# Optimization experiments

Measured on AMD Instinct MI355X. Metric: run time of the kernel, lower is better.

The kernel has to match this reference:

```python
import jax, jax.numpy as jnp
import numpy as np

NH, DH = 16, 64          # n_head, d_head
CH = NH + DH             # 80
RQ, RK, RV = 6, 2, 2
ROPE_BASE = 10000.0


def _rotary(b, cache_len):
    # b: [B, T, R, DH]; rotates the d-factor exactly as the torch Rotary module
    T = b.shape[1]
    inv_freq = (1.0 / ROPE_BASE) ** (jnp.arange(0, DH, 2, dtype=jnp.float32) / DH)
    t = jnp.arange(T, dtype=jnp.float32) + cache_len
    freqs = jnp.outer(t, inv_freq)                      # [T, DH/2]
    cos = freqs[None, :, None, :].astype(b.dtype)
    sin = jnp.sin(freqs)[None, :, None, :].astype(b.dtype)
    cos = jnp.cos(freqs)[None, :, None, :].astype(b.dtype)
    x1, x2 = jnp.split(b, 2, axis=3)
    return jnp.concatenate([x1 * cos + x2 * sin, -x1 * sin + x2 * cos], axis=3)


def setup_inputs() -> dict:
    key = jax.random.key(0)
    k1, k2, k3, k4 = jax.random.split(key, 4)
    B, T, D = 2, 2048, 1024
    x = jax.random.normal(k1, (B, T, D), dtype=jnp.float32)
    # xavier-uniform-like scale for factor projections
    s_q = float(np.sqrt(6.0 / (D + CH)))
    s_o = float(np.sqrt(6.0 / (D + D)))
    W_abq = jax.random.uniform(k2, (RQ * CH, D), minval=-s_q, maxval=s_q, dtype=jnp.float32)
    W_abkv = jax.random.uniform(k3, ((RK + RV) * CH, D), minval=-s_q, maxval=s_q, dtype=jnp.float32)
    W_o = jax.random.uniform(k4, (D, D), minval=-s_o, maxval=s_o, dtype=jnp.float32)
    return {"x": x, "W_abq": W_abq, "W_abkv": W_abkv, "W_o": W_o}


def reference(x, W_abq, W_abkv, W_o):
    B, T, D = x.shape
    # low-rank factor projections
    abq = (x @ W_abq.T).reshape(B, T, RQ, CH)
    a_q, b_q = abq[..., :NH], abq[..., NH:]            # [B,T,RQ,NH], [B,T,RQ,DH]
    abkv = (x @ W_abkv.T).reshape(B, T, RK + RV, CH)
    a_kv = abkv[..., :NH]
    b_kv = _rotary(abkv[..., NH:], cache_len=0)        # RoPE applied to K/V d-factors only
    a_k, b_k = a_kv[:, :, :RK], b_kv[:, :, :RK]
    a_v, b_v = a_kv[:, :, RK:], b_kv[:, :, RK:]
    # tensor-product reconstruction of Q/K/V
    q = jnp.einsum('btrh,btrd->bthd', a_q, b_q) / RQ
    k = jnp.einsum('btrh,btrd->bthd', a_k, b_k) / RK
    v = jnp.einsum('btrh,btrd->bthd', a_v, b_v) / RV
    # causal attention (flex_attention default scale = 1/sqrt(dh))
    scale = 1.0 / jnp.sqrt(jnp.asarray(DH, dtype=q.dtype))
    scores = jnp.einsum('bqhd,bkhd->bhqk', q, k) * scale
    causal = jnp.tril(jnp.ones((T, T), dtype=bool))
    scores = jnp.where(causal[None, None], scores, jnp.finfo(scores.dtype).min)
    attn = jax.nn.softmax(scores, axis=-1)
    y = jnp.einsum('bhqk,bkhd->bqhd', attn, v).reshape(B, T, D)
    return y @ W_o.T
```

## Files before the change

kernel.cpp:

```cpp
#include <hip/hip_runtime.h>
#include <hip/hip_bf16.h>
#include <math.h>

#define NHEADS 16
#define DHEAD  64
#define CHDIM  80
#define RQn    6
#define RKn    2
#define RVn    2
#define BB     2
#define TT     2048
#define DDim   1024
#define NQK    800

using frag16 = __attribute__((ext_vector_type(8))) short;
using f32x4  = __attribute__((ext_vector_type(4))) float;
using f32x16 = __attribute__((ext_vector_type(16))) float;

#define AS1(p) ((const __attribute__((address_space(1))) unsigned int*)(p))
#define AS3(p) ((__attribute__((address_space(3))) unsigned int*)(p))

static __device__ __forceinline__ unsigned short bf16_bits(float f) {
    __hip_bfloat16 h = __float2bfloat16(f);
    return *(unsigned short*)&h;
}
static __device__ __forceinline__ unsigned int pk2(float a, float b) {
    return ((unsigned int)bf16_bits(b) << 16) | (unsigned int)bf16_bits(a);
}

__global__ __launch_bounds__(256) void cvt_all(
    const float* __restrict__ x, const float* __restrict__ wq,
    const float* __restrict__ wk, const float* __restrict__ wo,
    __hip_bfloat16* __restrict__ xb, __hip_bfloat16* __restrict__ wqk,
    __hip_bfloat16* __restrict__ wob)
{
    int bid = blockIdx.x;
    const float* src; __hip_bfloat16* dst; int n4;
    if (bid < 4096)      { src = x;  dst = xb;            n4 = 1048576; }
    else if (bid < 4576) { bid -= 4096; src = wq; dst = wqk;           n4 = 122880; }
    else if (bid < 4896) { bid -= 4576; src = wk; dst = wqk + 491520;  n4 = 81920; }
    else                 { bid -= 4896; src = wo; dst = wob;           n4 = 262144; }
    int i = bid * 256 + threadIdx.x;
    if (i < n4) {
        float4 v = *(const float4*)&src[i * 4];
        ushort4 o;
        o.x = bf16_bits(v.x); o.y = bf16_bits(v.y);
        o.z = bf16_bits(v.z); o.w = bf16_bits(v.w);
        *(ushort4*)&dst[i * 4] = o;
    }
}

__global__ __launch_bounds__(256) void gemm_bf16(
    const __hip_bfloat16* __restrict__ A, const __hip_bfloat16* __restrict__ W,
    float* __restrict__ C, int M, int N, int K)
{
    __shared__ __hip_bfloat16 Asl[2][128 * 64];
    __shared__ __hip_bfloat16 Bsl[2][128 * 64];
    const int tid = threadIdx.x;
    const int w = tid >> 6, lane = tid & 63;
    const int l16 = lane & 15, quad = lane >> 4;
    const int wr = w >> 1, wc = w & 1;
    const int bm = blockIdx.y * 128, bn = blockIdx.x * 128;

    int rS[4], cS[4], rBS[4];
    #pragma unroll
    for (int j = 0; j < 4; j++) {
        int L = (w * 4 + j) * 64 + lane;
        rS[j] = L >> 3;
        cS[j] = (L & 7) ^ (rS[j] & 7);
        int rb = bn + rS[j];
        rBS[j] = (rb < N) ? rb : (N - 1);
    }

    f32x4 acc[4][4];
    #pragma unroll
    for (int mt = 0; mt < 4; mt++)
        #pragma unroll
        for (int nt = 0; nt < 4; nt++)
            acc[mt][nt] = (f32x4){0.f, 0.f, 0.f, 0.f};

    const int nK = K >> 6;
    #pragma unroll
    for (int j = 0; j < 4; j++) {
        const __hip_bfloat16* ga = A + (size_t)(bm + rS[j]) * K + cS[j] * 8;
        const __hip_bfloat16* gb = W + (size_t)rBS[j] * K + cS[j] * 8;
        __builtin_amdgcn_global_load_lds(AS1(ga), AS3(&Asl[0][(w * 4 + j) * 512]), 16, 0, 0);
        __builtin_amdgcn_global_load_lds(AS1(gb), AS3(&Bsl[0][(w * 4 + j) * 512]), 16, 0, 0);
    }

    for (int kk = 0; kk < nK; kk++) {
        const int cur = kk & 1;
        __syncthreads();
        if (kk + 1 < nK) {
            const int k1 = (kk + 1) * 64;
            #pragma unroll
            for (int j = 0; j < 4; j++) {
                const __hip_bfloat16* ga = A + (size_t)(bm + rS[j]) * K + k1 + cS[j] * 8;
                const __hip_bfloat16* gb = W + (size_t)rBS[j] * K + k1 + cS[j] * 8;
                __builtin_amdgcn_global_load_lds(AS1(ga), AS3(&Asl[cur ^ 1][(w * 4 + j) * 512]), 16, 0, 0);
                __builtin_amdgcn_global_load_lds(AS1(gb), AS3(&Bsl[cur ^ 1][(w * 4 + j) * 512]), 16, 0, 0);
            }
        }
        #pragma unroll
        for (int ks = 0; ks < 2; ks++) {
            frag16 af[4], bf[4];
            #pragma unroll
            for (int mt = 0; mt < 4; mt++) {
                int r = wr * 64 + mt * 16 + l16;
                af[mt] = *(const frag16*)&Asl[cur][r * 64 + (((ks * 4 + quad) ^ (r & 7)) * 8)];
            }
            #pragma unroll
            for (int nt = 0; nt < 4; nt++) {
                int r = wc * 64 + nt * 16 + l16;
                bf[nt] = *(const frag16*)&Bsl[cur][r * 64 + (((ks * 4 + quad) ^ (r & 7)) * 8)];
            }
            #pragma unroll
            for (int mt = 0; mt < 4; mt++)
                #pragma unroll
                for (int nt = 0; nt < 4; nt++)
                    acc[mt][nt] = __builtin_amdgcn_mfma_f32_16x16x32_bf16(af[mt], bf[nt], acc[mt][nt], 0, 0, 0);
        }
    }
    #pragma unroll
    for (int mt = 0; mt < 4; mt++) {
        #pragma unroll
        for (int reg = 0; reg < 4; reg++) {
            int row = bm + wr * 64 + mt * 16 + quad * 4 + reg;
            #pragma unroll
            for (int nt = 0; nt < 4; nt++) {
                int col = bn + wc * 64 + nt * 16 + l16;
                if (col < N) C[(size_t)row * N + col] = acc[mt][nt][reg];
            }
        }
    }
}

__global__ __launch_bounds__(256) void qkv_kernel(
    const float* __restrict__ ab,
    __hip_bfloat16* __restrict__ q, __hip_bfloat16* __restrict__ k,
    __hip_bfloat16* __restrict__ vT)
{
    const int tok0 = blockIdx.x * 4;
    const int w = threadIdx.x >> 6;
    const int d = threadIdx.x & 63;
    const int token = tok0 + w;
    const int b = token / TT;
    const int t = token % TT;
    __shared__ float sq[4][RQn * CHDIM];
    __shared__ float skv[4][(RKn + RVn) * CHDIM];
    __shared__ __align__(8) __hip_bfloat16 vbuf[NHEADS][DHEAD][4];
    const float* aq  = ab + (size_t)token * NQK;
    const float* akv = aq + 480;
    for (int i = d; i < RQn * CHDIM; i += 64) sq[w][i] = aq[i];
    for (int i = d; i < (RKn + RVn) * CHDIM; i += 64) skv[w][i] = akv[i];
    const int i32 = d & 31;
    float inv_freq = powf(10000.0f, -(float)i32 / 32.0f);
    float fr = (float)t * inv_freq;
    float c = cosf(fr), s = sinf(fr);
    float rot[4];
    #pragma unroll
    for (int r = 0; r < 4; r++) {
        float x1 = skv[w][r * CHDIM + NHEADS + i32];
        float x2 = skv[w][r * CHDIM + NHEADS + 32 + i32];
        rot[r] = (d < 32) ? (x1 * c + x2 * s) : (-x1 * s + x2 * c);
    }
    float bqv[RQn];
    #pragma unroll
    for (int r = 0; r < RQn; r++) bqv[r] = sq[w][r * CHDIM + NHEADS + d];
    #pragma unroll
    for (int h = 0; h < NHEADS; h++) {
        float accq = 0.0f;
        #pragma unroll
        for (int r = 0; r < RQn; r++)
            accq += sq[w][r * CHDIM + h] * bqv[r];
        q[((size_t)(b * NHEADS + h) * TT + t) * DHEAD + d] = __float2bfloat16(accq * (0.125f / 6.0f));
        float acck = 0.0f, accv = 0.0f;
        #pragma unroll
        for (int r = 0; r < RKn; r++)
            acck += skv[w][r * CHDIM + h] * rot[r];
        #pragma unroll
        for (int r = 0; r < RVn; r++)
            accv += skv[w][(RKn + r) * CHDIM + h] * rot[RKn + r];
        k[((size_t)(b * NHEADS + h) * TT + t) * DHEAD + d] = __float2bfloat16(acck * 0.5f);
        vbuf[h][d][w] = __float2bfloat16(accv * 0.5f);
    }
    __syncthreads();
    const int t0 = tok0 % TT;
    const int b0 = tok0 / TT;
    for (int row = threadIdx.x; row < NHEADS * DHEAD; row += 256) {
        int h = row >> 6, dd = row & 63;
        *(uint2*)&vT[((size_t)(b0 * NHEADS + h) * DHEAD + dd) * TT + t0] =
            *(const uint2*)&vbuf[h][dd][0];
    }
}

__global__ __launch_bounds__(256, 3) void flash_mfma(
    const __hip_bfloat16* __restrict__ q, const __hip_bfloat16* __restrict__ k,
    const __hip_bfloat16* __restrict__ vT, __hip_bfloat16* __restrict__ y)
{
    const int L = blockIdx.x;
    const int bh = L & 31;
    const int rr = L >> 5;
    const int qt = (L < 256) ? rr : (15 - (rr & 7));
    const int b = bh >> 4, h = bh & 15;
    const int tid = threadIdx.x;
    const int w = tid >> 6;
    const int lane = tid & 63;
    const int l31 = lane & 31;
    const int hi = lane >> 5;
    const int xi = l31 & 7;
    const int paddr = (lane ^ 32) << 2;

    __shared__ __align__(16) __hip_bfloat16 KsF[2][4096];
    __shared__ __align__(16) __hip_bfloat16 VsF[2][4096];

    const size_t base = (size_t)bh * TT * DHEAD;
    const __hip_bfloat16* qb = q + base;
    const __hip_bfloat16* kb = k + base;
    const __hip_bfloat16* vb = vT + base;

    const int qrow0 = qt * 128 + w * 32;
    const int qlane = qrow0 + l31;
    const int ktd = qrow0 >> 6;

    int offK[2], offV[2];
    #pragma unroll
    for (int j = 0; j < 2; j++) {
        int Lc = w * 128 + j * 64 + lane;
        int r = Lc >> 3, c8 = Lc & 7, g8 = c8 ^ (r & 7);
        offK[j] = r * 64 + g8 * 8;
        offV[j] = r * TT + g8 * 8;
    }

    frag16 qB[4];
    #pragma unroll
    for (int kt4 = 0; kt4 < 4; kt4++)
        qB[kt4] = *(const frag16*)&qb[(size_t)qlane * DHEAD + kt4 * 16 + hi * 8];

    f32x16 O0 = {}, O1 = {};
    float lpart = 0.0f;

    const int nkt = 2 * qt + 2;
    #pragma unroll
    for (int j = 0; j < 2; j++) {
        __builtin_amdgcn_global_load_lds(AS1(kb + offK[j]),
                                         AS3(&KsF[0][w * 1024 + j * 512]), 16, 0, 0);
        __builtin_amdgcn_global_load_lds(AS1(vb + offV[j]),
                                         AS3(&VsF[0][w * 1024 + j * 512]), 16, 0, 0);
    }

    for (int kt = 0; kt < nkt; kt++) {
        const int cur = kt & 1;
        __syncthreads();
        if (kt + 1 < nkt) {
            #pragma unroll
            for (int j = 0; j < 2; j++) {
                __builtin_amdgcn_global_load_lds(AS1(kb + (size_t)(kt + 1) * 4096 + offK[j]),
                                                 AS3(&KsF[cur ^ 1][w * 1024 + j * 512]), 16, 0, 0);
                __builtin_amdgcn_global_load_lds(AS1(vb + (size_t)(kt + 1) * 64 + offV[j]),
                                                 AS3(&VsF[cur ^ 1][w * 1024 + j * 512]), 16, 0, 0);
            }
        }
        if (kt <= ktd) {
            const __hip_bfloat16* Kc = KsF[cur];
            const __hip_bfloat16* Vc = VsF[cur];
            f32x16 ST0 = {}, ST1 = {};
            #pragma unroll
            for (int kt4 = 0; kt4 < 4; kt4++) {
                int c8 = kt4 * 2 + hi;
                frag16 kf0 = *(const frag16*)&Kc[l31 * 64 + ((c8 ^ xi) * 8)];
                frag16 kf1 = *(const frag16*)&Kc[(32 + l31) * 64 + ((c8 ^ xi) * 8)];
                ST0 = __builtin_amdgcn_mfma_f32_32x32x16_bf16(kf0, qB[kt4], ST0, 0, 0, 0);
                ST1 = __builtin_amdgcn_mfma_f32_32x32x16_bf16(kf1, qB[kt4], ST1, 0, 0, 0);
            }
            float* s0 = (float*)&ST0;
            float* s1 = (float*)&ST1;
            if (kt == ktd) {
                int kb0 = kt * 64 + 4 * hi;
                #pragma unroll
                for (int reg = 0; reg < 16; reg++) {
                    int rowc = (reg & 3) + 8 * (reg >> 2);
                    if (kb0 + rowc > qlane)      s0[reg] = -1e30f;
                    if (kb0 + 32 + rowc > qlane) s1[reg] = -1e30f;
                }
            }
            #pragma unroll
            for (int reg = 0; reg < 16; reg++) {
                float p0 = __expf(s0[reg]);
                float p1 = __expf(s1[reg]);
                s0[reg] = p0; s1[reg] = p1;
                lpart += p0 + p1;
            }
            frag16 Pf[4];
            #pragma unroll
            for (int k2 = 0; k2 < 4; k2++) {
                const float* sF = (k2 >= 2) ? s1 : s0;
                const int bs = 8 * (k2 & 1);
                unsigned int u0a = pk2(sF[bs + 0], sF[bs + 1]);
                unsigned int u0b = pk2(sF[bs + 2], sF[bs + 3]);
                unsigned int u1a = pk2(sF[bs + 4], sF[bs + 5]);
                unsigned int u1b = pk2(sF[bs + 6], sF[bs + 7]);
                unsigned int r0a = (unsigned int)__builtin_amdgcn_ds_bpermute(paddr, (int)u0a);
                unsigned int r0b = (unsigned int)__builtin_amdgcn_ds_bpermute(paddr, (int)u0b);
                unsigned int r1a = (unsigned int)__builtin_amdgcn_ds_bpermute(paddr, (int)u1a);
                unsigned int r1b = (unsigned int)__builtin_amdgcn_ds_bpermute(paddr, (int)u1b);
                union { frag16 f; unsigned int u[4]; } pf;
                pf.u[0] = hi ? r1a : u0a;
                pf.u[1] = hi ? r1b : u0b;
                pf.u[2] = hi ? u1a : r0a;
                pf.u[3] = hi ? u1b : r0b;
                Pf[k2] = pf.f;
            }
            #pragma unroll
            for (int k2 = 0; k2 < 4; k2++) {
                int c8 = k2 * 2 + hi;
                frag16 vf0 = *(const frag16*)&Vc[l31 * 64 + ((c8 ^ xi) * 8)];
                frag16 vf1 = *(const frag16*)&Vc[(32 + l31) * 64 + ((c8 ^ xi) * 8)];
                O0 = __builtin_amdgcn_mfma_f32_32x32x16_bf16(vf0, Pf[k2], O0, 0, 0, 0);
                O1 = __builtin_amdgcn_mfma_f32_32x32x16_bf16(vf1, Pf[k2], O1, 0, 0, 0);
            }
        }
    }

    float lother = __int_as_float(__builtin_amdgcn_ds_bpermute(paddr, __float_as_int(lpart)));
    float inv = 1.0f / (lpart + lother);
    float* o0 = (float*)&O0;
    float* o1 = (float*)&O1;
    __hip_bfloat16* yp = y + ((size_t)(b * TT + qlane)) * DDim + h * DHEAD;
    #pragma unroll
    for (int g = 0; g < 4; g++) {
        int d0 = 8 * g + 4 * hi;
        uint2 pa, pb;
        pa.x = pk2(o0[4*g+0] * inv, o0[4*g+1] * inv);
        pa.y = pk2(o0[4*g+2] * inv, o0[4*g+3] * inv);
        pb.x = pk2(o1[4*g+0] * inv, o1[4*g+1] * inv);
        pb.y = pk2(o1[4*g+2] * inv, o1[4*g+3] * inv);
        *(uint2*)&yp[d0] = pa;
        *(uint2*)&yp[32 + d0] = pb;
    }
}

extern "C" void kernel_launch(void* const* d_in, const int* in_sizes, int n_in,
                              void* d_out, int out_size, void* d_ws, size_t ws_size,
                              hipStream_t stream) {
    const float* x      = (const float*)d_in[0];
    const float* W_abq  = (const float*)d_in[1];
    const float* W_abkv = (const float*)d_in[2];
    const float* W_o    = (const float*)d_in[3];
    float* out = (float*)d_out;

    char* ws = (char*)d_ws;
    __hip_bfloat16* xb   = (__hip_bfloat16*)ws;  ws += (size_t)4194304 * 2;
    __hip_bfloat16* wqk  = (__hip_bfloat16*)ws;  ws += (size_t)NQK * 1024 * 2;
    __hip_bfloat16* wo_b = (__hip_bfloat16*)ws;  ws += (size_t)1048576 * 2;
    float* abqkv = (float*)ws;                   ws += (size_t)4096 * NQK * 4;
    __hip_bfloat16* qb = (__hip_bfloat16*)ws;    ws += (size_t)4194304 * 2;
    __hip_bfloat16* kb = (__hip_bfloat16*)ws;    ws += (size_t)4194304 * 2;
    __hip_bfloat16* vT = (__hip_bfloat16*)ws;    ws += (size_t)4194304 * 2;
    __hip_bfloat16* yb = (__hip_bfloat16*)ws;    ws += (size_t)4194304 * 2;

    cvt_all<<<dim3(5920), dim3(256), 0, stream>>>(x, W_abq, W_abkv, W_o, xb, wqk, wo_b);
    gemm_bf16<<<dim3(7, 32), dim3(256), 0, stream>>>(xb, wqk, abqkv, 4096, NQK, 1024);
    qkv_kernel<<<dim3(1024), dim3(256), 0, stream>>>(abqkv, qb, kb, vT);
    flash_mfma<<<dim3(512), dim3(256), 0, stream>>>(qb, kb, vT, yb);
    gemm_bf16<<<dim3(8, 32), dim3(256), 0, stream>>>(yb, wo_b, out, 4096, 1024, 1024);
}
```

Measured before the change: 186.7 us.

## Pair causal q-tiles and split heavy tile across blocks with combine pass

Restructures causal flash attention work distribution: each block pairs a light q-tile with part of a heavy q-tile (15-qt), sharing K/V tile loads, and the heavy tile's key range is split between two blocks whose partial outputs and row sums are written as fp32 and merged by a new combine kernel. The aim is to balance work per block so every block runs a similar number of K/V steps, and to reuse each loaded K/V tile for two query tiles. In exchange it adds fp32 partial-output traffic, an extra kernel launch, and lower occupancy from the reduced launch bound.

```diff
diff --git a/kernel.cpp b/kernel.cpp
--- a/kernel.cpp
+++ b/kernel.cpp
@@ -194,14 +194,82 @@
     }
 }
 
-__global__ __launch_bounds__(256, 3) void flash_mfma(
+static __device__ __forceinline__ void attn_tile(
+    const __hip_bfloat16* __restrict__ Kc, const __hip_bfloat16* __restrict__ Vc,
+    const frag16 qB[4], f32x16& O0, f32x16& O1, float& lpart,
+    const int l31, const int hi, const int xi, const int paddr,
+    const bool domask, const int kb0, const int qlane)
+{
+    f32x16 ST0 = {}, ST1 = {};
+    #pragma unroll
+    for (int kt4 = 0; kt4 < 4; kt4++) {
+        int c8 = kt4 * 2 + hi;
+        frag16 kf0 = *(const frag16*)&Kc[l31 * 64 + ((c8 ^ xi) * 8)];
+        frag16 kf1 = *(const frag16*)&Kc[(32 + l31) * 64 + ((c8 ^ xi) * 8)];
+        ST0 = __builtin_amdgcn_mfma_f32_32x32x16_bf16(kf0, qB[kt4], ST0, 0, 0, 0);
+        ST1 = __builtin_amdgcn_mfma_f32_32x32x16_bf16(kf1, qB[kt4], ST1, 0, 0, 0);
+    }
+    float* s0 = (float*)&ST0;
+    float* s1 = (float*)&ST1;
+    if (domask) {
+        int kbq = kb0 + 4 * hi;
+        #pragma unroll
+        for (int reg = 0; reg < 16; reg++) {
+            int rowc = (reg & 3) + 8 * (reg >> 2);
+            if (kbq + rowc > qlane)      s0[reg] = -1e30f;
+            if (kbq + 32 + rowc > qlane) s1[reg] = -1e30f;
+        }
+    }
+    #pragma unroll
+    for (int reg = 0; reg < 16; reg++) {
+        float p0 = __expf(s0[reg]);
+        float p1 = __expf(s1[reg]);
+        s0[reg] = p0; s1[reg] = p1;
+        lpart += p0 + p1;
+    }
+    frag16 Pf[4];
+    #pragma unroll
+    for (int k2 = 0; k2 < 4; k2++) {
+        const float* sF = (k2 >= 2) ? s1 : s0;
+        const int bs = 8 * (k2 & 1);
+        unsigned int u0a = pk2(sF[bs + 0], sF[bs + 1]);
+        unsigned int u0b = pk2(sF[bs + 2], sF[bs + 3]);
+        unsigned int u1a = pk2(sF[bs + 4], sF[bs + 5]);
+        unsigned int u1b = pk2(sF[bs + 6], sF[bs + 7]);
+        unsigned int r0a = (unsigned int)__builtin_amdgcn_ds_bpermute(paddr, (int)u0a);
+        unsigned int r0b = (unsigned int)__builtin_amdgcn_ds_bpermute(paddr, (int)u0b);
+        unsigned int r1a = (unsigned int)__builtin_amdgcn_ds_bpermute(paddr, (int)u1a);
+        unsigned int r1b = (unsigned int)__builtin_amdgcn_ds_bpermute(paddr, (int)u1b);
+        union { frag16 f; unsigned int u[4]; } pf;
+        pf.u[0] = hi ? r1a : u0a;
+        pf.u[1] = hi ? r1b : u0b;
+        pf.u[2] = hi ? u1a : r0a;
+        pf.u[3] = hi ? u1b : r0b;
+        Pf[k2] = pf.f;
+    }
+    #pragma unroll
+    for (int k2 = 0; k2 < 4; k2++) {
+        int c8 = k2 * 2 + hi;
+        frag16 vf0 = *(const frag16*)&Vc[l31 * 64 + ((c8 ^ xi) * 8)];
+        frag16 vf1 = *(const frag16*)&Vc[(32 + l31) * 64 + ((c8 ^ xi) * 8)];
+        O0 = __builtin_amdgcn_mfma_f32_32x32x16_bf16(vf0, Pf[k2], O0, 0, 0, 0);
+        O1 = __builtin_amdgcn_mfma_f32_32x32x16_bf16(vf1, Pf[k2], O1, 0, 0, 0);
+    }
+}
+
+__global__ __launch_bounds__(256, 2) void flash_mfma(
     const __hip_bfloat16* __restrict__ q, const __hip_bfloat16* __restrict__ k,
-    const __hip_bfloat16* __restrict__ vT, __hip_bfloat16* __restrict__ y)
-{
-    const int L = blockIdx.x;
-    const int bh = L & 31;
-    const int rr = L >> 5;
-    const int qt = (L < 256) ? rr : (15 - (rr & 7));
+    const __hip_bfloat16* __restrict__ vT, __hip_bfloat16* __restrict__ y,
+    float* __restrict__ Op, float* __restrict__ Lp)
+{
+    const int g = blockIdx.x;
+    const int bh = g & 31;
+    const int pr = g >> 5;
+    const int qthalf = pr & 7;
+    const int part = pr >> 3;
+    const int qt_lo = qthalf, qt_hi = 15 - qthalf;
+    const int nlo = 2 * qt_lo + 2;
+    const int S = 17 - nlo;
     const int b = bh >> 4, h = bh & 15;
     const int tid = threadIdx.x;
     const int w = tid >> 6;
@@ -219,9 +287,13 @@
     const __hip_bfloat16* kb = k + base;
     const __hip_bfloat16* vb = vT + base;
 
-    const int qrow0 = qt * 128 + w * 32;
-    const int qlane = qrow0 + l31;
-    const int ktd = qrow0 >> 6;
+    const int ktd_lo = 2 * qt_lo + (w >> 1);
+    const int ktd_hi = 2 * qt_hi + (w >> 1);
+    const int qlane_lo = qt_lo * 128 + w * 32 + l31;
+    const int qlane_hi = qt_hi * 128 + w * 32 + l31;
+
+    const int k0off  = part ? S : 0;
+    const int nsteps = part ? 17 : ((nlo > S) ? nlo : S);
 
     int offK[2], offV[2];
     #pragma unroll
@@ -232,111 +304,120 @@
         offV[j] = r * TT + g8 * 8;
     }
 
-    frag16 qB[4];
+    frag16 qB_hi[4], qB_lo[4];
     #pragma unroll
     for (int kt4 = 0; kt4 < 4; kt4++)
-        qB[kt4] = *(const frag16*)&qb[(size_t)qlane * DHEAD + kt4 * 16 + hi * 8];
-
-    f32x16 O0 = {}, O1 = {};
-    float lpart = 0.0f;
-
-    const int nkt = 2 * qt + 2;
+        qB_hi[kt4] = *(const frag16*)&qb[(size_t)qlane_hi * DHEAD + kt4 * 16 + hi * 8];
+    if (part == 0) {
+        #pragma unroll
+        for (int kt4 = 0; kt4 < 4; kt4++)
+            qB_lo[kt4] = *(const frag16*)&qb[(size_t)qlane_lo * DHEAD + kt4 * 16 + hi * 8];
+    }
+
+    f32x16 Olo0 = {}, Olo1 = {}, Ohi0 = {}, Ohi1 = {};
+    float l_lo = 0.0f, l_hi = 0.0f;
+
     #pragma unroll
     for (int j = 0; j < 2; j++) {
-        __builtin_amdgcn_global_load_lds(AS1(kb + offK[j]),
+        __builtin_amdgcn_global_load_lds(AS1(kb + (size_t)k0off * 4096 + offK[j]),
                                          AS3(&KsF[0][w * 1024 + j * 512]), 16, 0, 0);
-        __builtin_amdgcn_global_load_lds(AS1(vb + offV[j]),
+        __builtin_amdgcn_global_load_lds(AS1(vb + (size_t)k0off * 64 + offV[j]),
                                          AS3(&VsF[0][w * 1024 + j * 512]), 16, 0, 0);
     }
 
-    for (int kt = 0; kt < nkt; kt++) {
+    for (int kt = 0; kt < nsteps; kt++) {
         const int cur = kt & 1;
         __syncthreads();
-        if (kt + 1 < nkt) {
+        if (kt + 1 < nsteps) {
+            const int phys1 = k0off + kt + 1;
             #pragma unroll
             for (int j = 0; j < 2; j++) {
-                __builtin_amdgcn_global_load_lds(AS1(kb + (size_t)(kt + 1) * 4096 + offK[j]),
+                __builtin_amdgcn_global_load_lds(AS1(kb + (size_t)phys1 * 4096 + offK[j]),
                                                  AS3(&KsF[cur ^ 1][w * 1024 + j * 512]), 16, 0, 0);
-                __builtin_amdgcn_global_load_lds(AS1(vb + (size_t)(kt + 1) * 64 + offV[j]),
+                __builtin_amdgcn_global_load_lds(AS1(vb + (size_t)phys1 * 64 + offV[j]),
                                                  AS3(&VsF[cur ^ 1][w * 1024 + j * 512]), 16, 0, 0);
             }
         }
-        if (kt <= ktd) {
-            const __hip_bfloat16* Kc = KsF[cur];
-            const __hip_bfloat16* Vc = VsF[cur];
-            f32x16 ST0 = {}, ST1 = {};
-            #pragma unroll
-            for (int kt4 = 0; kt4 < 4; kt4++) {
-                int c8 = kt4 * 2 + hi;
-                frag16 kf0 = *(const frag16*)&Kc[l31 * 64 + ((c8 ^ xi) * 8)];
-                frag16 kf1 = *(const frag16*)&Kc[(32 + l31) * 64 + ((c8 ^ xi) * 8)];
-                ST0 = __builtin_amdgcn_mfma_f32_32x32x16_bf16(kf0, qB[kt4], ST0, 0, 0, 0);
-                ST1 = __builtin_amdgcn_mfma_f32_32x32x16_bf16(kf1, qB[kt4], ST1, 0, 0, 0);
-            }
-            float* s0 = (float*)&ST0;
-            float* s1 = (float*)&ST1;
-            if (kt == ktd) {
-                int kb0 = kt * 64 + 4 * hi;
-                #pragma unroll
-                for (int reg = 0; reg < 16; reg++) {
-                    int rowc = (reg & 3) + 8 * (reg >> 2);
-                    if (kb0 + rowc > qlane)      s0[reg] = -1e30f;
-                    if (kb0 + 32 + rowc > qlane) s1[reg] = -1e30f;
-                }
-            }
-            #pragma unroll
-            for (int reg = 0; reg < 16; reg++) {
-                float p0 = __expf(s0[reg]);
-                float p1 = __expf(s1[reg]);
-                s0[reg] = p0; s1[reg] = p1;
-                lpart += p0 + p1;
-            }
-            frag16 Pf[4];
-            #pragma unroll
-            for (int k2 = 0; k2 < 4; k2++) {
-                const float* sF = (k2 >= 2) ? s1 : s0;
-                const int bs = 8 * (k2 & 1);
-                unsigned int u0a = pk2(sF[bs + 0], sF[bs + 1]);
-                unsigned int u0b = pk2(sF[bs + 2], sF[bs + 3]);
-                unsigned int u1a = pk2(sF[bs + 4], sF[bs + 5]);
-                unsigned int u1b = pk2(sF[bs + 6], sF[bs + 7]);
-                unsigned int r0a = (unsigned int)__builtin_amdgcn_ds_bpermute(paddr, (int)u0a);
-                unsigned int r0b = (unsigned int)__builtin_amdgcn_ds_bpermute(paddr, (int)u0b);
-                unsigned int r1a = (unsigned int)__builtin_amdgcn_ds_bpermute(paddr, (int)u1a);
-                unsigned int r1b = (unsigned int)__builtin_amdgcn_ds_bpermute(paddr, (int)u1b);
-                union { frag16 f; unsigned int u[4]; } pf;
-                pf.u[0] = hi ? r1a : u0a;
-                pf.u[1] = hi ? r1b : u0b;
-                pf.u[2] = hi ? u1a : r0a;
-                pf.u[3] = hi ? u1b : r0b;
-                Pf[k2] = pf.f;
-            }
-            #pragma unroll
-            for (int k2 = 0; k2 < 4; k2++) {
-                int c8 = k2 * 2 + hi;
-                frag16 vf0 = *(const frag16*)&Vc[l31 * 64 + ((c8 ^ xi) * 8)];
-                frag16 vf1 = *(const frag16*)&Vc[(32 + l31) * 64 + ((c8 ^ xi) * 8)];
-                O0 = __builtin_amdgcn_mfma_f32_32x32x16_bf16(vf0, Pf[k2], O0, 0, 0, 0);
-                O1 = __builtin_amdgcn_mfma_f32_32x32x16_bf16(vf1, Pf[k2], O1, 0, 0, 0);
-            }
-        }
-    }
-
-    float lother = __int_as_float(__builtin_amdgcn_ds_bpermute(paddr, __float_as_int(lpart)));
-    float inv = 1.0f / (lpart + lother);
-    float* o0 = (float*)&O0;
-    float* o1 = (float*)&O1;
-    __hip_bfloat16* yp = y + ((size_t)(b * TT + qlane)) * DDim + h * DHEAD;
-    #pragma unroll
-    for (int g = 0; g < 4; g++) {
-        int d0 = 8 * g + 4 * hi;
-        uint2 pa, pb;
-        pa.x = pk2(o0[4*g+0] * inv, o0[4*g+1] * inv);
-        pa.y = pk2(o0[4*g+2] * inv, o0[4*g+3] * inv);
-        pb.x = pk2(o1[4*g+0] * inv, o1[4*g+1] * inv);
-        pb.y = pk2(o1[4*g+2] * inv, o1[4*g+3] * inv);
-        *(uint2*)&yp[d0] = pa;
-        *(uint2*)&yp[32 + d0] = pb;
+        const __hip_bfloat16* Kc = KsF[cur];
+        const __hip_bfloat16* Vc = VsF[cur];
+        if (part == 0) {
+            if (kt <= ktd_lo)
+                attn_tile(Kc, Vc, qB_lo, Olo0, Olo1, l_lo, l31, hi, xi, paddr,
+                          kt == ktd_lo, kt * 64, qlane_lo);
+            if (kt < S)
+                attn_tile(Kc, Vc, qB_hi, Ohi0, Ohi1, l_hi, l31, hi, xi, paddr,
+                          false, 0, qlane_hi);
+        } else {
+            const int phys = S + kt;
+            if (phys <= ktd_hi)
+                attn_tile(Kc, Vc, qB_hi, Ohi0, Ohi1, l_hi, l31, hi, xi, paddr,
+                          phys == ktd_hi, phys * 64, qlane_hi);
+        }
+    }
+
+    if (part == 0) {
+        float lother = __int_as_float(__builtin_amdgcn_ds_bpermute(paddr, __float_as_int(l_lo)));
+        float inv = 1.0f / (l_lo + lother);
+        float* o0 = (float*)&Olo0;
+        float* o1 = (float*)&Olo1;
+        __hip_bfloat16* yp = y + ((size_t)(b * TT + qlane_lo)) * DDim + h * DHEAD;
+        #pragma unroll
+        for (int gg = 0; gg < 4; gg++) {
+            int d0 = 8 * gg + 4 * hi;
+            uint2 pa, pb;
+            pa.x = pk2(o0[4*gg+0] * inv, o0[4*gg+1] * inv);
+            pa.y = pk2(o0[4*gg+2] * inv, o0[4*gg+3] * inv);
+            pb.x = pk2(o1[4*gg+0] * inv, o1[4*gg+1] * inv);
+            pb.y = pk2(o1[4*gg+2] * inv, o1[4*gg+3] * inv);
+            *(uint2*)&yp[d0] = pa;
+            *(uint2*)&yp[32 + d0] = pb;
+        }
+    }
+    {
+        float lother = __int_as_float(__builtin_amdgcn_ds_bpermute(paddr, __float_as_int(l_hi)));
+        float ltot = l_hi + lother;
+        const int slot = bh * 8 + qthalf;
+        const int rloc = w * 32 + l31;
+        float* Od = Op + ((size_t)part * 256 + slot) * 8192 + (size_t)rloc * 64;
+        float* o0 = (float*)&Ohi0;
+        float* o1 = (float*)&Ohi1;
+        #pragma unroll
+        for (int gg = 0; gg < 4; gg++) {
+            int d0 = 8 * gg + 4 * hi;
+            *(float4*)&Od[d0]      = (float4){o0[4*gg+0], o0[4*gg+1], o0[4*gg+2], o0[4*gg+3]};
+            *(float4*)&Od[32 + d0] = (float4){o1[4*gg+0], o1[4*gg+1], o1[4*gg+2], o1[4*gg+3]};
+        }
+        if (hi == 0) Lp[part * 32768 + slot * 128 + rloc] = ltot;
+    }
+}
+
+__global__ __launch_bounds__(256) void combine(
+    const float* __restrict__ Op, const float* __restrict__ Lp,
+    __hip_bfloat16* __restrict__ y)
+{
+    int idx = blockIdx.x * 256 + threadIdx.x;
+    int slot = idx >> 7, row = idx & 127;
+    int bh = slot >> 3, qthalf = slot & 7;
+    int b = bh >> 4, h = bh & 15;
+    int qrow = (15 - qthalf) * 128 + row;
+    float l0 = Lp[slot * 128 + row];
+    float l1 = Lp[32768 + slot * 128 + row];
+    float inv = 1.0f / (l0 + l1);
+    const float* p0 = Op + (size_t)(slot * 128 + row) * 64;
+    const float* p1 = p0 + 2097152;
+    __hip_bfloat16* yp = y + ((size_t)(b * TT + qrow)) * DDim + h * DHEAD;
+    #pragma unroll
+    for (int c = 0; c < 64; c += 8) {
+        float4 a0 = *(const float4*)&p0[c];
+        float4 a1 = *(const float4*)&p0[c + 4];
+        float4 b0 = *(const float4*)&p1[c];
+        float4 b1 = *(const float4*)&p1[c + 4];
+        uint4 o;
+        o.x = pk2((a0.x + b0.x) * inv, (a0.y + b0.y) * inv);
+        o.y = pk2((a0.z + b0.z) * inv, (a0.w + b0.w) * inv);
+        o.z = pk2((a1.x + b1.x) * inv, (a1.y + b1.y) * inv);
+        o.w = pk2((a1.z + b1.z) * inv, (a1.w + b1.w) * inv);
+        *(uint4*)&yp[c] = o;
     }
 }
 
@@ -358,10 +439,13 @@
     __hip_bfloat16* kb = (__hip_bfloat16*)ws;    ws += (size_t)4194304 * 2;
     __hip_bfloat16* vT = (__hip_bfloat16*)ws;    ws += (size_t)4194304 * 2;
     __hip_bfloat16* yb = (__hip_bfloat16*)ws;    ws += (size_t)4194304 * 2;
+    float* Op = (float*)ws;                      ws += (size_t)2 * 2097152 * 4;
+    float* Lp = (float*)ws;                      ws += (size_t)2 * 32768 * 4;
 
     cvt_all<<<dim3(5920), dim3(256), 0, stream>>>(x, W_abq, W_abkv, W_o, xb, wqk, wo_b);
     gemm_bf16<<<dim3(7, 32), dim3(256), 0, stream>>>(xb, wqk, abqkv, 4096, NQK, 1024);
     qkv_kernel<<<dim3(1024), dim3(256), 0, stream>>>(abqkv, qb, kb, vT);
-    flash_mfma<<<dim3(512), dim3(256), 0, stream>>>(qb, kb, vT, yb);
+    flash_mfma<<<dim3(512), dim3(256), 0, stream>>>(qb, kb, vT, yb, Op, Lp);
+    combine<<<dim3(128), dim3(256), 0, stream>>>(Op, Lp, yb);
     gemm_bf16<<<dim3(8, 32), dim3(256), 0, stream>>>(yb, wo_b, out, 4096, 1024, 1024);
 }
```

Measured after the change: 183.8 us. No clear change (-1.6%).
